# Kernel optimization log

Hardware: AMD Instinct MI355X
Metric: run time of the kernel (lower is better)

Reference implementation:

```python
import jax, jax.numpy as jnp
import numpy as np

N_NODES = 50000
N_EDGES = 800000
IN_DIM = 512
HID = 128
HEADS = 8
HEAD_DIM = HID // HEADS  # 16
N_LAYERS = 3
N_CLASSES = 8


def layer_norm(x, g, b, eps=1e-5):
    mu = jnp.mean(x, axis=-1, keepdims=True)
    var = jnp.mean((x - mu) ** 2, axis=-1, keepdims=True)
    return (x - mu) * jax.lax.rsqrt(var + eps) * g + b


def gat_layer(h, W, a_src, a_dst, bias, src, dst):
    # h: [N, HID]; W: [HID, HEADS*HEAD_DIM]; a_src/a_dst: [HEADS, HEAD_DIM]
    N = h.shape[0]
    hp = (h @ W).reshape(N, HEADS, HEAD_DIM)  # per-head projections
    e_s = jnp.einsum('nhc,hc->nh', hp, a_src)  # [N, H]
    e_d = jnp.einsum('nhc,hc->nh', hp, a_dst)
    logits = jax.nn.leaky_relu(e_s[src] + e_d[dst], negative_slope=0.2)  # [E, H]
    # segment softmax over incoming edges of each dst node
    m = jax.ops.segment_max(logits, dst, num_segments=N)
    p = jnp.exp(logits - m[dst])
    denom = jax.ops.segment_sum(p, dst, num_segments=N)
    alpha = p / (denom[dst] + 1e-16)  # [E, H]
    msg = hp[src] * alpha[:, :, None]  # [E, H, C]
    out = jax.ops.segment_sum(msg, dst, num_segments=N)  # [N, H, C]
    return out.reshape(N, HEADS * HEAD_DIM) + bias


def setup_inputs() -> dict:
    key = jax.random.key(0)
    ks = jax.random.split(key, 32)
    s = 0.05
    inp = {}
    inp['x'] = jax.random.normal(ks[0], (N_NODES, IN_DIM), dtype=jnp.float32)
    inp['edge_src'] = jax.random.randint(ks[1], (N_EDGES,), 0, N_NODES, dtype=jnp.int32)
    inp['edge_dst'] = jax.random.randint(ks[2], (N_EDGES,), 0, N_NODES, dtype=jnp.int32)
    # input projection
    inp['W_in'] = jax.random.normal(ks[3], (IN_DIM, HID)) * s
    inp['b_in'] = jnp.zeros((HID,))
    inp['g_in'] = jnp.ones((HID,))
    inp['be_in'] = jnp.zeros((HID,))
    # stacked GAT layer params
    inp['Wc'] = jax.random.normal(ks[4], (N_LAYERS, HID, HEADS * HEAD_DIM)) * s
    inp['a_src'] = jax.random.normal(ks[5], (N_LAYERS, HEADS, HEAD_DIM)) * s
    inp['a_dst'] = jax.random.normal(ks[6], (N_LAYERS, HEADS, HEAD_DIM)) * s
    inp['bc'] = jnp.zeros((N_LAYERS, HID))
    inp['gc'] = jnp.ones((N_LAYERS, HID))
    inp['bec'] = jnp.zeros((N_LAYERS, HID))
    # classifier
    inp['W1'] = jax.random.normal(ks[7], (HID, HID // 2)) * s
    inp['b1'] = jnp.zeros((HID // 2,))
    inp['g1'] = jnp.ones((HID // 2,))
    inp['be1'] = jnp.zeros((HID // 2,))
    inp['W2'] = jax.random.normal(ks[8], (HID // 2, HID // 4)) * s
    inp['b2'] = jnp.zeros((HID // 4,))
    inp['g2'] = jnp.ones((HID // 4,))
    inp['be2'] = jnp.zeros((HID // 4,))
    inp['W3'] = jax.random.normal(ks[9], (HID // 4, N_CLASSES)) * s
    inp['b3'] = jnp.zeros((N_CLASSES,))
    return inp


def reference(x, W_in, b_in, g_in, be_in, Wc, a_src, a_dst, bc, gc, bec,
              W1, b1, g1, be1, W2, b2, g2, be2, W3, b3, edge_src, edge_dst):
    N = x.shape[0]
    # PyG GATConv adds self-loops by default
    loops = jnp.arange(N, dtype=edge_src.dtype)
    src = jnp.concatenate([edge_src, loops])
    dst = jnp.concatenate([edge_dst, loops])
    # input projection (dropout is identity in eval)
    h = jax.nn.relu(layer_norm(x @ W_in + b_in, g_in, be_in))
    for i in range(N_LAYERS):
        residual = h
        h = gat_layer(h, Wc[i], a_src[i], a_dst[i], bc[i], src, dst)
        h = jax.nn.relu(layer_norm(h, gc[i], bec[i]))
        if i > 0:
            h = h + residual
    # classifier head
    h = jax.nn.relu(layer_norm(h @ W1 + b1, g1, be1))
    h = jax.nn.relu(layer_norm(h @ W2 + b2, g2, be2))
    return h @ W3 + b3
```

## Files before the change

### kernel.cpp

```cpp
#include <hip/hip_runtime.h>
#include <math.h>

#define N_NODES 50000
#define N_EDGES 800000
#define IN_DIM 512
#define HID 128
#define HEADS 8
#define HEAD_DIM 16
#define N_LAYERS 3
#define N_CLASSES 8
#define LOG2E 1.4426950408889634f
#define NBLK 196

typedef __attribute__((ext_vector_type(8))) short short8;
typedef __attribute__((ext_vector_type(4))) short short4v;
typedef __attribute__((ext_vector_type(4))) float f32x4;

__device__ inline unsigned short f2bf(float f) {
  unsigned u = __float_as_uint(f);
  u = (u + 0x7fffu + ((u >> 16) & 1u)) >> 16;
  return (unsigned short)u;
}
__device__ inline float bflo(unsigned u) { return __uint_as_float(u << 16); }
__device__ inline float bfhi(unsigned u) { return __uint_as_float(u & 0xffff0000u); }

__global__ __launch_bounds__(256) void k_prep(
    const float* __restrict__ W_in, const float* __restrict__ Wc,
    const float* __restrict__ W1, const float* __restrict__ W2,
    const float* __restrict__ W3,
    unsigned short* __restrict__ Wt_in, unsigned short* __restrict__ Wt_c,
    unsigned short* __restrict__ W1t, unsigned short* __restrict__ W2t,
    unsigned short* __restrict__ W3t, int* __restrict__ degcur) {
  int i = blockIdx.x * blockDim.x + threadIdx.x;
  if (i < 2 * N_NODES) degcur[i] = 0;
  if (i < IN_DIM * HID) {
    int c = i >> 9, k = i & 511;
    Wt_in[i] = f2bf(W_in[k * HID + c]);
  }
  if (i < N_LAYERS * HID * HID) {
    int l = i >> 14, r = i & 16383, c = r >> 7, k = r & 127;
    Wt_c[i] = f2bf(Wc[l * HID * HID + k * HID + c]);
  }
  if (i < 64 * 128) {
    int c = i >> 7, k = i & 127;
    W1t[i] = f2bf(W1[k * 64 + c]);
  }
  if (i < 32 * 64) {
    int c = i >> 6, k = i & 63;
    W2t[i] = f2bf(W2[k * 32 + c]);
  }
  if (i < 16 * 32) {
    int c = i >> 5, k = i & 31;
    W3t[i] = (c < 8) ? f2bf(W3[k * N_CLASSES + c]) : 0;
  }
}

template <int K>
__device__ inline void gemm_mainloop(const float* __restrict__ A, size_t row0,
                                     const unsigned short* __restrict__ Wt,
                                     unsigned short* lds_a, unsigned short* lds_b,
                                     f32x4 acc[8]) {
  const int tid = threadIdx.x;
  const int lane = tid & 63, wid = tid >> 6;
#pragma unroll
  for (int f = 0; f < 8; ++f)
#pragma unroll
    for (int j = 0; j < 4; ++j) acc[f][j] = 0.f;

  for (int kb = 0; kb < K; kb += 64) {
#pragma unroll
    for (int j = 0; j < 4; ++j) {
      int i = tid + j * 256;
      int r = i >> 4, kq = (i & 15) * 4;
      size_t rg = row0 + r;
      if (rg >= N_NODES) rg = N_NODES - 1;
      float4 v = *(const float4*)(A + rg * K + kb + kq);
      short4v b4;
      b4[0] = (short)f2bf(v.x); b4[1] = (short)f2bf(v.y);
      b4[2] = (short)f2bf(v.z); b4[3] = (short)f2bf(v.w);
      int idx = (r * 64 + kq) ^ ((r & 7) << 3);
      *(short4v*)&lds_a[idx] = b4;
    }
#pragma unroll
    for (int j = 0; j < 4; ++j) {
      int i = tid + j * 256;
      int c = i >> 3, kq = (i & 7) * 8;
      short8 w = *(const short8*)(Wt + (size_t)c * K + kb + kq);
      int idx = (c * 64 + kq) ^ ((c & 7) << 3);
      *(short8*)&lds_b[idx] = w;
    }
    __syncthreads();

    int arow = wid * 16 + (lane & 15);
    int kq8 = (lane >> 4) * 8;
    short8 a0 = *(short8*)&lds_a[(arow * 64 + kq8) ^ ((arow & 7) << 3)];
    short8 a1 = *(short8*)&lds_a[(arow * 64 + 32 + kq8) ^ ((arow & 7) << 3)];
#pragma unroll
    for (int f = 0; f < 8; ++f) {
      int c = f * 16 + (lane & 15);
      short8 b0 = *(short8*)&lds_b[(c * 64 + kq8) ^ ((c & 7) << 3)];
      short8 b1 = *(short8*)&lds_b[(c * 64 + 32 + kq8) ^ ((c & 7) << 3)];
      acc[f] = __builtin_amdgcn_mfma_f32_16x16x32_bf16(a0, b0, acc[f], 0, 0, 0);
      acc[f] = __builtin_amdgcn_mfma_f32_16x16x32_bf16(a1, b1, acc[f], 0, 0, 0);
    }
    __syncthreads();
  }
}

__global__ __launch_bounds__(256) void k_gemm_in(
    const float* __restrict__ x, const unsigned short* __restrict__ Wt,
    const float* __restrict__ b, const float* __restrict__ g,
    const float* __restrict__ be, float* __restrict__ h0) {
  __shared__ unsigned short lds_a[64 * 64];
  __shared__ unsigned short lds_b[128 * 64];
  f32x4 acc[8];
  size_t row0 = (size_t)blockIdx.x * 64;
  gemm_mainloop<IN_DIM>(x, row0, Wt, lds_a, lds_b, acc);

  int lane = threadIdx.x & 63, wid = threadIdx.x >> 6;
  int cbase = lane & 15;
  float s[4] = {0.f, 0.f, 0.f, 0.f}, q[4] = {0.f, 0.f, 0.f, 0.f};
  float gg[8], bb[8];
#pragma unroll
  for (int f = 0; f < 8; ++f) {
    int c = f * 16 + cbase;
    float bias = b[c];
    gg[f] = g[c]; bb[f] = be[c];
#pragma unroll
    for (int j = 0; j < 4; ++j) {
      float v = acc[f][j] + bias;
      acc[f][j] = v;
      s[j] += v; q[j] += v * v;
    }
  }
#pragma unroll
  for (int off = 8; off >= 1; off >>= 1)
#pragma unroll
    for (int j = 0; j < 4; ++j) {
      s[j] += __shfl_xor(s[j], off);
      q[j] += __shfl_xor(q[j], off);
    }
#pragma unroll
  for (int j = 0; j < 4; ++j) {
    size_t row = row0 + wid * 16 + (lane >> 4) * 4 + j;
    if (row < N_NODES) {
      float mu = s[j] * (1.f / 128.f);
      float var = q[j] * (1.f / 128.f) - mu * mu;
      float rs = rsqrtf(var + 1e-5f);
#pragma unroll
      for (int f = 0; f < 8; ++f) {
        float y = (acc[f][j] - mu) * rs * gg[f] + bb[f];
        h0[row * HID + f * 16 + cbase] = fmaxf(y, 0.f);
      }
    }
  }
}

__global__ __launch_bounds__(256) void k_gemm_gat(
    const float* __restrict__ h, const unsigned short* __restrict__ Wt,
    const float* __restrict__ asrc, const float* __restrict__ adst,
    unsigned short* __restrict__ hp_bf, float* __restrict__ es,
    float* __restrict__ ed) {
  __shared__ unsigned short lds_a[64 * 64];
  __shared__ unsigned short lds_b[128 * 64];
  f32x4 acc[8];
  size_t row0 = (size_t)blockIdx.x * 64;
  gemm_mainloop<HID>(h, row0, Wt, lds_a, lds_b, acc);

  int lane = threadIdx.x & 63, wid = threadIdx.x >> 6;
  int cbase = lane & 15;
#pragma unroll
  for (int f = 0; f < 8; ++f) {
    float av = asrc[f * 16 + cbase], bv = adst[f * 16 + cbase];
    float eS[4], eD[4];
#pragma unroll
    for (int j = 0; j < 4; ++j) { eS[j] = acc[f][j] * av; eD[j] = acc[f][j] * bv; }
#pragma unroll
    for (int off = 8; off >= 1; off >>= 1)
#pragma unroll
      for (int j = 0; j < 4; ++j) {
        eS[j] += __shfl_xor(eS[j], off);
        eD[j] += __shfl_xor(eD[j], off);
      }
#pragma unroll
    for (int j = 0; j < 4; ++j) {
      size_t row = row0 + wid * 16 + (lane >> 4) * 4 + j;
      if (row < N_NODES) {
        hp_bf[row * HID + f * 16 + cbase] = f2bf(acc[f][j]);
        if (cbase == 0) {
          es[row * HEADS + f] = eS[j] * LOG2E;
          ed[row * HEADS + f] = eD[j] * LOG2E;
        }
      }
    }
  }
}

__global__ void k_count(const int* __restrict__ dst, int* __restrict__ deg) {
  int e = blockIdx.x * blockDim.x + threadIdx.x;
  if (e < N_EDGES) atomicAdd(&deg[dst[e]], 1);
}

__global__ __launch_bounds__(256) void k_scan_local(
    const int* __restrict__ deg, int* __restrict__ startv,
    int* __restrict__ blocksum) {
  __shared__ int wsum[4];
  int tid = threadIdx.x, lane = tid & 63, wid = tid >> 6;
  int n = blockIdx.x * 256 + tid;
  int d = (n < N_NODES) ? deg[n] : 0;
  int v = d;
#pragma unroll
  for (int off = 1; off < 64; off <<= 1) {
    int t = __shfl_up(v, off);
    if (lane >= off) v += t;
  }
  if (lane == 63) wsum[wid] = v;
  __syncthreads();
  int prefix = 0;
  for (int w = 0; w < wid; ++w) prefix += wsum[w];
  int excl = prefix + v - d;
  if (n < N_NODES) startv[n] = excl;
  if (tid == 255) blocksum[blockIdx.x] = excl + d;
}

__global__ __launch_bounds__(256) void k_scan_block(
    const int* __restrict__ blocksum, int* __restrict__ blockoffs) {
  __shared__ int wsum[4];
  int tid = threadIdx.x, lane = tid & 63, wid = tid >> 6;
  int d = (tid < NBLK) ? blocksum[tid] : 0;
  int v = d;
#pragma unroll
  for (int off = 1; off < 64; off <<= 1) {
    int t = __shfl_up(v, off);
    if (lane >= off) v += t;
  }
  if (lane == 63) wsum[wid] = v;
  __syncthreads();
  int prefix = 0;
  for (int w = 0; w < wid; ++w) prefix += wsum[w];
  if (tid < NBLK) blockoffs[tid] = prefix + v - d;
}

__global__ __launch_bounds__(256) void k_scan_add(
    int* __restrict__ startv, const int* __restrict__ blockoffs) {
  int n = blockIdx.x * blockDim.x + threadIdx.x;
  if (n < N_NODES) startv[n] += blockoffs[blockIdx.x];
}

__global__ void k_scatter(const int* __restrict__ src, const int* __restrict__ dst,
                          const int* __restrict__ start, int* __restrict__ cur,
                          int* __restrict__ col) {
  int e = blockIdx.x * blockDim.x + threadIdx.x;
  if (e < N_EDGES) {
    int d = dst[e];
    int pos = start[d] + atomicAdd(&cur[d], 1);
    col[pos] = src[e];
  }
}

__global__ __launch_bounds__(256) void k_gat_agg(
    const unsigned short* __restrict__ hp_bf, const float* __restrict__ es,
    const float* __restrict__ ed, const int* __restrict__ start,
    const int* __restrict__ deg, const int* __restrict__ col,
    const float* __restrict__ bc, const float* __restrict__ gc,
    const float* __restrict__ bec, const float* __restrict__ h_res,
    float* __restrict__ h_out, int use_res) {
  int lane = threadIdx.x & 63;
  int n = blockIdx.x * 4 + (threadIdx.x >> 6);
  if (n >= N_NODES) return;
  int head = lane >> 3;
  int sub = lane & 7;
  int hbase = head * 8;
  const unsigned* hpu = (const unsigned*)hp_bf;

  float edv = ed[(size_t)n * HEADS + head];
  float z0 = es[(size_t)n * HEADS + head] + edv;
  z0 = fmaxf(z0, 0.2f * z0);
  float p0 = exp2f(z0);
  unsigned su = hpu[(size_t)n * 64 + lane];

  float den0 = p0, ax0 = p0 * bflo(su), ay0 = p0 * bfhi(su);
  float den1 = 0.f, ax1 = 0.f, ay1 = 0.f;

  int s0 = start[n], s1 = s0 + deg[n];
  int nb = (s1 - s0) >> 3;
  int base = s0;
  int se = 0;
  float p = 0.f;
  if (nb > 0) {
    se = col[base + sub];
    float z = es[(size_t)se * HEADS + head] + edv;
    z = fmaxf(z, 0.2f * z);
    p = exp2f(z);
  }
  for (int t = 0; t < nb; ++t) {
    int seN = 0;
    bool more = (t + 1 < nb);
    if (more) seN = col[base + 8 + sub];
#pragma unroll
    for (int k = 0; k < 8; k += 2) {
      float pk0 = __shfl(p, hbase + k);
      float pk1 = __shfl(p, hbase + k + 1);
      int sk0 = __shfl(se, k);
      int sk1 = __shfl(se, k + 1);
      unsigned h0 = hpu[(size_t)sk0 * 64 + lane];
      unsigned h1 = hpu[(size_t)sk1 * 64 + lane];
      den0 += pk0;
      ax0 = fmaf(pk0, bflo(h0), ax0);
      ay0 = fmaf(pk0, bfhi(h0), ay0);
      den1 += pk1;
      ax1 = fmaf(pk1, bflo(h1), ax1);
      ay1 = fmaf(pk1, bfhi(h1), ay1);
    }
    if (more) {
      float zN = es[(size_t)seN * HEADS + head] + edv;
      zN = fmaxf(zN, 0.2f * zN);
      p = exp2f(zN);
      se = seN;
    }
    base += 8;
  }
  int rem = s1 - base;
  if (rem > 0) {
    int e = base + (sub < rem ? sub : rem - 1);
    int set = col[e];
    float z = es[(size_t)set * HEADS + head] + edv;
    z = fmaxf(z, 0.2f * z);
    float pt = (sub < rem) ? exp2f(z) : 0.f;
    for (int k = 0; k < rem; ++k) {
      float pk = __shfl(pt, hbase + k);
      int sk = __shfl(set, k);
      unsigned hk = hpu[(size_t)sk * 64 + lane];
      den0 += pk;
      ax0 = fmaf(pk, bflo(hk), ax0);
      ay0 = fmaf(pk, bfhi(hk), ay0);
    }
  }
  float den = den0 + den1 + 1e-16f;
  float rden = 1.f / den;
  float v0 = (ax0 + ax1) * rden + bc[2 * lane];
  float v1 = (ay0 + ay1) * rden + bc[2 * lane + 1];

  float s = v0 + v1, q = v0 * v0 + v1 * v1;
#pragma unroll
  for (int off = 32; off >= 1; off >>= 1) {
    s += __shfl_xor(s, off);
    q += __shfl_xor(q, off);
  }
  float mu = s * (1.f / 128.f);
  float var = q * (1.f / 128.f) - mu * mu;
  float rs = rsqrtf(var + 1e-5f);
  float y0 = fmaxf((v0 - mu) * rs * gc[2 * lane] + bec[2 * lane], 0.f);
  float y1 = fmaxf((v1 - mu) * rs * gc[2 * lane + 1] + bec[2 * lane + 1], 0.f);
  if (use_res) {
    float2 r = ((const float2*)h_res)[(size_t)n * 64 + lane];
    y0 += r.x; y1 += r.y;
  }
  ((float2*)h_out)[(size_t)n * 64 + lane] = make_float2(y0, y1);
}

__global__ __launch_bounds__(256) void k_head_mfma(
    const float* __restrict__ h,
    const unsigned short* __restrict__ W1t, const float* __restrict__ b1,
    const float* __restrict__ g1, const float* __restrict__ be1,
    const unsigned short* __restrict__ W2t, const float* __restrict__ b2,
    const float* __restrict__ g2, const float* __restrict__ be2,
    const unsigned short* __restrict__ W3t, const float* __restrict__ b3,
    float* __restrict__ out) {
  __shared__ unsigned short lds_a[64 * 128];
  __shared__ unsigned short lds_b1[64 * 128];
  __shared__ unsigned short lds_h1[64 * 64];
  __shared__ unsigned short lds_b2[32 * 64];
  __shared__ unsigned short lds_h2[64 * 32];
  __shared__ unsigned short lds_b3[16 * 32];
  int tid = threadIdx.x, lane = tid & 63, wid = tid >> 6;
  size_t row0 = (size_t)blockIdx.x * 64;

#pragma unroll
  for (int jj = 0; jj < 8; ++jj) {
    int i = tid + jj * 256;
    int r = i >> 5, kq = (i & 31) * 4;
    size_t rg = row0 + r;
    if (rg >= N_NODES) rg = N_NODES - 1;
    float4 v = *(const float4*)(h + rg * HID + kq);
    short4v b4;
    b4[0] = (short)f2bf(v.x); b4[1] = (short)f2bf(v.y);
    b4[2] = (short)f2bf(v.z); b4[3] = (short)f2bf(v.w);
    int idx = (r * 128 + kq) ^ ((r & 7) << 3);
    *(short4v*)&lds_a[idx] = b4;
  }
#pragma unroll
  for (int jj = 0; jj < 4; ++jj) {
    int i = tid + jj * 256;
    int c = i >> 4, kq = (i & 15) * 8;
    short8 w = *(const short8*)(W1t + c * 128 + kq);
    int idx = (c * 128 + kq) ^ ((c & 7) << 3);
    *(short8*)&lds_b1[idx] = w;
  }
  {
    int c = tid >> 3, kq = (tid & 7) * 8;
    if (c < 32) {
      short8 w = *(const short8*)(W2t + c * 64 + kq);
      int idx = (c * 64 + kq) ^ ((c & 7) << 3);
      *(short8*)&lds_b2[idx] = w;
    }
  }
  if (tid < 64) {
    int c = tid >> 2, kq = (tid & 3) * 8;
    short8 w = *(const short8*)(W3t + c * 32 + kq);
    int idx = (c * 32 + kq) ^ ((c & 3) << 3);
    *(short8*)&lds_b3[idx] = w;
  }
  __syncthreads();

  int arow = wid * 16 + (lane & 15);
  int kq8 = (lane >> 4) * 8;
  int cbase = lane & 15;

  f32x4 acc1[4];
#pragma unroll
  for (int f = 0; f < 4; ++f)
#pragma unroll
    for (int j = 0; j < 4; ++j) acc1[f][j] = 0.f;
  {
    short8 a0 = *(short8*)&lds_a[(arow * 128 + kq8) ^ ((arow & 7) << 3)];
    short8 a1 = *(short8*)&lds_a[(arow * 128 + 32 + kq8) ^ ((arow & 7) << 3)];
    short8 a2 = *(short8*)&lds_a[(arow * 128 + 64 + kq8) ^ ((arow & 7) << 3)];
    short8 a3 = *(short8*)&lds_a[(arow * 128 + 96 + kq8) ^ ((arow & 7) << 3)];
#pragma unroll
    for (int f = 0; f < 4; ++f) {
      int c = f * 16 + cbase;
      short8 b0 = *(short8*)&lds_b1[(c * 128 + kq8) ^ ((c & 7) << 3)];
      short8 bb1 = *(short8*)&lds_b1[(c * 128 + 32 + kq8) ^ ((c & 7) << 3)];
      short8 b2v = *(short8*)&lds_b1[(c * 128 + 64 + kq8) ^ ((c & 7) << 3)];
      short8 b3v = *(short8*)&lds_b1[(c * 128 + 96 + kq8) ^ ((c & 7) << 3)];
      acc1[f] = __builtin_amdgcn_mfma_f32_16x16x32_bf16(a0, b0, acc1[f], 0, 0, 0);
      acc1[f] = __builtin_amdgcn_mfma_f32_16x16x32_bf16(a1, bb1, acc1[f], 0, 0, 0);
      acc1[f] = __builtin_amdgcn_mfma_f32_16x16x32_bf16(a2, b2v, acc1[f], 0, 0, 0);
      acc1[f] = __builtin_amdgcn_mfma_f32_16x16x32_bf16(a3, b3v, acc1[f], 0, 0, 0);
    }
  }
  {
    float s[4] = {0, 0, 0, 0}, q[4] = {0, 0, 0, 0};
#pragma unroll
    for (int f = 0; f < 4; ++f) {
      int c = f * 16 + cbase;
      float bias = b1[c];
#pragma unroll
      for (int j = 0; j < 4; ++j) {
        float v = acc1[f][j] + bias;
        acc1[f][j] = v;
        s[j] += v; q[j] += v * v;
      }
    }
#pragma unroll
    for (int off = 8; off >= 1; off >>= 1)
#pragma unroll
      for (int j = 0; j < 4; ++j) {
        s[j] += __shfl_xor(s[j], off);
        q[j] += __shfl_xor(q[j], off);
      }
#pragma unroll
    for (int j = 0; j < 4; ++j) {
      int row = wid * 16 + (lane >> 4) * 4 + j;
      float mu = s[j] * (1.f / 64.f);
      float var = q[j] * (1.f / 64.f) - mu * mu;
      float rs = rsqrtf(var + 1e-5f);
#pragma unroll
      for (int f = 0; f < 4; ++f) {
        int c = f * 16 + cbase;
        float y = fmaxf((acc1[f][j] - mu) * rs * g1[c] + be1[c], 0.f);
        lds_h1[(row * 64 + c) ^ ((row & 7) << 3)] = f2bf(y);
      }
    }
  }
  __syncthreads();

  f32x4 acc2[2];
#pragma unroll
  for (int f = 0; f < 2; ++f)
#pragma unroll
    for (int j = 0; j < 4; ++j) acc2[f][j] = 0.f;
  {
    short8 a0 = *(short8*)&lds_h1[(arow * 64 + kq8) ^ ((arow & 7) << 3)];
    short8 a1 = *(short8*)&lds_h1[(arow * 64 + 32 + kq8) ^ ((arow & 7) << 3)];
#pragma unroll
    for (int f = 0; f < 2; ++f) {
      int c = f * 16 + cbase;
      short8 b0 = *(short8*)&lds_b2[(c * 64 + kq8) ^ ((c & 7) << 3)];
      short8 bb1 = *(short8*)&lds_b2[(c * 64 + 32 + kq8) ^ ((c & 7) << 3)];
      acc2[f] = __builtin_amdgcn_mfma_f32_16x16x32_bf16(a0, b0, acc2[f], 0, 0, 0);
      acc2[f] = __builtin_amdgcn_mfma_f32_16x16x32_bf16(a1, bb1, acc2[f], 0, 0, 0);
    }
  }
  {
    float s[4] = {0, 0, 0, 0}, q[4] = {0, 0, 0, 0};
#pragma unroll
    for (int f = 0; f < 2; ++f) {
      int c = f * 16 + cbase;
      float bias = b2[c];
#pragma unroll
      for (int j = 0; j < 4; ++j) {
        float v = acc2[f][j] + bias;
        acc2[f][j] = v;
        s[j] += v; q[j] += v * v;
      }
    }
#pragma unroll
    for (int off = 8; off >= 1; off >>= 1)
#pragma unroll
      for (int j = 0; j < 4; ++j) {
        s[j] += __shfl_xor(s[j], off);
        q[j] += __shfl_xor(q[j], off);
      }
#pragma unroll
    for (int j = 0; j < 4; ++j) {
      int row = wid * 16 + (lane >> 4) * 4 + j;
      float mu = s[j] * (1.f / 32.f);
      float var = q[j] * (1.f / 32.f) - mu * mu;
      float rs = rsqrtf(var + 1e-5f);
#pragma unroll
      for (int f = 0; f < 2; ++f) {
        int c = f * 16 + cbase;
        float y = fmaxf((acc2[f][j] - mu) * rs * g2[c] + be2[c], 0.f);
        lds_h2[(row * 32 + c) ^ ((row & 3) << 3)] = f2bf(y);
      }
    }
  }
  __syncthreads();

  f32x4 acc3;
#pragma unroll
  for (int j = 0; j < 4; ++j) acc3[j] = 0.f;
  {
    short8 a = *(short8*)&lds_h2[(arow * 32 + kq8) ^ ((arow & 3) << 3)];
    short8 b = *(short8*)&lds_b3[(cbase * 32 + kq8) ^ ((cbase & 3) << 3)];
    acc3 = __builtin_amdgcn_mfma_f32_16x16x32_bf16(a, b, acc3, 0, 0, 0);
  }
  if (cbase < N_CLASSES) {
    float bias = b3[cbase];
#pragma unroll
    for (int j = 0; j < 4; ++j) {
      size_t row = row0 + wid * 16 + (lane >> 4) * 4 + j;
      if (row < N_NODES) out[row * N_CLASSES + cbase] = acc3[j] + bias;
    }
  }
}

extern "C" void kernel_launch(void* const* d_in, const int* in_sizes, int n_in,
                              void* d_out, int out_size, void* d_ws, size_t ws_size,
                              hipStream_t stream) {
  const float* x     = (const float*)d_in[0];
  const int*   esrc  = (const int*)d_in[1];
  const int*   edst  = (const int*)d_in[2];
  const float* W_in  = (const float*)d_in[3];
  const float* b_in  = (const float*)d_in[4];
  const float* g_in  = (const float*)d_in[5];
  const float* be_in = (const float*)d_in[6];
  const float* Wc    = (const float*)d_in[7];
  const float* a_src = (const float*)d_in[8];
  const float* a_dst = (const float*)d_in[9];
  const float* bc    = (const float*)d_in[10];
  const float* gc    = (const float*)d_in[11];
  const float* bec   = (const float*)d_in[12];
  const float* W1    = (const float*)d_in[13];
  const float* b1    = (const float*)d_in[14];
  const float* g1    = (const float*)d_in[15];
  const float* be1   = (const float*)d_in[16];
  const float* W2    = (const float*)d_in[17];
  const float* b2    = (const float*)d_in[18];
  const float* g2    = (const float*)d_in[19];
  const float* be2   = (const float*)d_in[20];
  const float* W3    = (const float*)d_in[21];
  const float* b3    = (const float*)d_in[22];

  float* ws = (float*)d_ws;
  const size_t NH = (size_t)N_NODES * HID;
  float* hA = ws;
  float* hB = hA + NH;
  float* es = hB + NH;
  float* ed = es + (size_t)N_NODES * HEADS;
  unsigned short* hp_bf = (unsigned short*)(ed + (size_t)N_NODES * HEADS);
  int* deg    = (int*)(hp_bf + NH);
  int* cur    = deg + N_NODES;
  int* startv = cur + N_NODES;
  int* blocksum  = startv + N_NODES;
  int* blockoffs = blocksum + NBLK;
  int* col    = blockoffs + NBLK;
  uintptr_t wp = (uintptr_t)(col + N_EDGES);
  wp = (wp + 15) & ~(uintptr_t)15;
  unsigned short* Wt_in = (unsigned short*)wp;
  unsigned short* Wt_c  = Wt_in + (size_t)IN_DIM * HID;
  unsigned short* W1t   = Wt_c + (size_t)N_LAYERS * HID * HID;
  unsigned short* W2t   = W1t + 64 * 128;
  unsigned short* W3t   = W2t + 32 * 64;

  k_prep<<<(2 * N_NODES + 255) / 256, 256, 0, stream>>>(
      W_in, Wc, W1, W2, W3, Wt_in, Wt_c, W1t, W2t, W3t, deg);

  k_gemm_in<<<(N_NODES + 63) / 64, 256, 0, stream>>>(x, Wt_in, b_in, g_in, be_in, hA);

  k_count<<<(N_EDGES + 255) / 256, 256, 0, stream>>>(edst, deg);
  k_scan_local<<<NBLK, 256, 0, stream>>>(deg, startv, blocksum);
  k_scan_block<<<1, 256, 0, stream>>>(blocksum, blockoffs);
  k_scan_add<<<NBLK, 256, 0, stream>>>(startv, blockoffs);
  k_scatter<<<(N_EDGES + 255) / 256, 256, 0, stream>>>(esrc, edst, startv, cur, col);

  float* hcur = hA;
  float* hnext = hB;
  for (int l = 0; l < N_LAYERS; ++l) {
    k_gemm_gat<<<(N_NODES + 63) / 64, 256, 0, stream>>>(
        hcur, Wt_c + (size_t)l * HID * HID,
        a_src + (size_t)l * HEADS * HEAD_DIM, a_dst + (size_t)l * HEADS * HEAD_DIM,
        hp_bf, es, ed);
    k_gat_agg<<<(N_NODES + 3) / 4, 256, 0, stream>>>(
        hp_bf, es, ed, startv, deg, col,
        bc + (size_t)l * HID, gc + (size_t)l * HID, bec + (size_t)l * HID,
        hcur, hnext, l > 0 ? 1 : 0);
    float* t = hcur; hcur = hnext; hnext = t;
  }

  k_head_mfma<<<(N_NODES + 63) / 64, 256, 0, stream>>>(
      hcur, W1t, b1, g1, be1, W2t, b2, g2, be2, W3t, b3, (float*)d_out);
}
```

Before: 338.3 us.

## Store hidden activations in bf16 between layers instead of fp32

Hidden-state buffers hA/hB become bf16 instead of fp32. The input GEMM, GAT aggregation and residual path write and read packed bf16, and the GAT GEMM and classifier head load bf16 directly into LDS without converting. This halves the bytes moved for inter-layer activations and removes the per-load fp32-to-bf16 conversion. In exchange, the residual stream now carries bf16 rounding, which loses some precision.

```diff
diff --git a/kernel.cpp b/kernel.cpp
--- a/kernel.cpp
+++ b/kernel.cpp
@@ -55,8 +55,8 @@
   }
 }
 
-template <int K>
-__device__ inline void gemm_mainloop(const float* __restrict__ A, size_t row0,
+template <int K, bool ABF>
+__device__ inline void gemm_mainloop(const void* __restrict__ Av, size_t row0,
                                      const unsigned short* __restrict__ Wt,
                                      unsigned short* lds_a, unsigned short* lds_b,
                                      f32x4 acc[8]) {
@@ -68,18 +68,33 @@
     for (int j = 0; j < 4; ++j) acc[f][j] = 0.f;
 
   for (int kb = 0; kb < K; kb += 64) {
-#pragma unroll
-    for (int j = 0; j < 4; ++j) {
-      int i = tid + j * 256;
-      int r = i >> 4, kq = (i & 15) * 4;
-      size_t rg = row0 + r;
-      if (rg >= N_NODES) rg = N_NODES - 1;
-      float4 v = *(const float4*)(A + rg * K + kb + kq);
-      short4v b4;
-      b4[0] = (short)f2bf(v.x); b4[1] = (short)f2bf(v.y);
-      b4[2] = (short)f2bf(v.z); b4[3] = (short)f2bf(v.w);
-      int idx = (r * 64 + kq) ^ ((r & 7) << 3);
-      *(short4v*)&lds_a[idx] = b4;
+    if (ABF) {
+      const unsigned short* A = (const unsigned short*)Av;
+#pragma unroll
+      for (int j = 0; j < 2; ++j) {
+        int i = tid + j * 256;
+        int r = i >> 3, kq = (i & 7) * 8;
+        size_t rg = row0 + r;
+        if (rg >= N_NODES) rg = N_NODES - 1;
+        short8 v = *(const short8*)(A + rg * K + kb + kq);
+        int idx = (r * 64 + kq) ^ ((r & 7) << 3);
+        *(short8*)&lds_a[idx] = v;
+      }
+    } else {
+      const float* A = (const float*)Av;
+#pragma unroll
+      for (int j = 0; j < 4; ++j) {
+        int i = tid + j * 256;
+        int r = i >> 4, kq = (i & 15) * 4;
+        size_t rg = row0 + r;
+        if (rg >= N_NODES) rg = N_NODES - 1;
+        float4 v = *(const float4*)(A + rg * K + kb + kq);
+        short4v b4;
+        b4[0] = (short)f2bf(v.x); b4[1] = (short)f2bf(v.y);
+        b4[2] = (short)f2bf(v.z); b4[3] = (short)f2bf(v.w);
+        int idx = (r * 64 + kq) ^ ((r & 7) << 3);
+        *(short4v*)&lds_a[idx] = b4;
+      }
     }
 #pragma unroll
     for (int j = 0; j < 4; ++j) {
@@ -110,12 +125,12 @@
 __global__ __launch_bounds__(256) void k_gemm_in(
     const float* __restrict__ x, const unsigned short* __restrict__ Wt,
     const float* __restrict__ b, const float* __restrict__ g,
-    const float* __restrict__ be, float* __restrict__ h0) {
+    const float* __restrict__ be, unsigned short* __restrict__ h0) {
   __shared__ unsigned short lds_a[64 * 64];
   __shared__ unsigned short lds_b[128 * 64];
   f32x4 acc[8];
   size_t row0 = (size_t)blockIdx.x * 64;
-  gemm_mainloop<IN_DIM>(x, row0, Wt, lds_a, lds_b, acc);
+  gemm_mainloop<IN_DIM, false>(x, row0, Wt, lds_a, lds_b, acc);
 
   int lane = threadIdx.x & 63, wid = threadIdx.x >> 6;
   int cbase = lane & 15;
@@ -150,14 +165,14 @@
 #pragma unroll
       for (int f = 0; f < 8; ++f) {
         float y = (acc[f][j] - mu) * rs * gg[f] + bb[f];
-        h0[row * HID + f * 16 + cbase] = fmaxf(y, 0.f);
+        h0[row * HID + f * 16 + cbase] = f2bf(fmaxf(y, 0.f));
       }
     }
   }
 }
 
 __global__ __launch_bounds__(256) void k_gemm_gat(
-    const float* __restrict__ h, const unsigned short* __restrict__ Wt,
+    const unsigned short* __restrict__ h, const unsigned short* __restrict__ Wt,
     const float* __restrict__ asrc, const float* __restrict__ adst,
     unsigned short* __restrict__ hp_bf, float* __restrict__ es,
     float* __restrict__ ed) {
@@ -165,7 +180,7 @@
   __shared__ unsigned short lds_b[128 * 64];
   f32x4 acc[8];
   size_t row0 = (size_t)blockIdx.x * 64;
-  gemm_mainloop<HID>(h, row0, Wt, lds_a, lds_b, acc);
+  gemm_mainloop<HID, true>(h, row0, Wt, lds_a, lds_b, acc);
 
   int lane = threadIdx.x & 63, wid = threadIdx.x >> 6;
   int cbase = lane & 15;
@@ -263,8 +278,8 @@
     const float* __restrict__ ed, const int* __restrict__ start,
     const int* __restrict__ deg, const int* __restrict__ col,
     const float* __restrict__ bc, const float* __restrict__ gc,
-    const float* __restrict__ bec, const float* __restrict__ h_res,
-    float* __restrict__ h_out, int use_res) {
+    const float* __restrict__ bec, const unsigned* __restrict__ h_res,
+    unsigned* __restrict__ h_out, int use_res) {
   int lane = threadIdx.x & 63;
   int n = blockIdx.x * 4 + (threadIdx.x >> 6);
   if (n >= N_NODES) return;
@@ -353,14 +368,14 @@
   float y0 = fmaxf((v0 - mu) * rs * gc[2 * lane] + bec[2 * lane], 0.f);
   float y1 = fmaxf((v1 - mu) * rs * gc[2 * lane + 1] + bec[2 * lane + 1], 0.f);
   if (use_res) {
-    float2 r = ((const float2*)h_res)[(size_t)n * 64 + lane];
-    y0 += r.x; y1 += r.y;
-  }
-  ((float2*)h_out)[(size_t)n * 64 + lane] = make_float2(y0, y1);
+    unsigned r = h_res[(size_t)n * 64 + lane];
+    y0 += bflo(r); y1 += bfhi(r);
+  }
+  h_out[(size_t)n * 64 + lane] = (unsigned)f2bf(y0) | ((unsigned)f2bf(y1) << 16);
 }
 
 __global__ __launch_bounds__(256) void k_head_mfma(
-    const float* __restrict__ h,
+    const unsigned short* __restrict__ h,
     const unsigned short* __restrict__ W1t, const float* __restrict__ b1,
     const float* __restrict__ g1, const float* __restrict__ be1,
     const unsigned short* __restrict__ W2t, const float* __restrict__ b2,
@@ -377,17 +392,14 @@
   size_t row0 = (size_t)blockIdx.x * 64;
 
 #pragma unroll
-  for (int jj = 0; jj < 8; ++jj) {
+  for (int jj = 0; jj < 4; ++jj) {
     int i = tid + jj * 256;
-    int r = i >> 5, kq = (i & 31) * 4;
+    int r = i >> 4, kq = (i & 15) * 8;
     size_t rg = row0 + r;
     if (rg >= N_NODES) rg = N_NODES - 1;
-    float4 v = *(const float4*)(h + rg * HID + kq);
-    short4v b4;
-    b4[0] = (short)f2bf(v.x); b4[1] = (short)f2bf(v.y);
-    b4[2] = (short)f2bf(v.z); b4[3] = (short)f2bf(v.w);
+    short8 v = *(const short8*)(h + rg * HID + kq);
     int idx = (r * 128 + kq) ^ ((r & 7) << 3);
-    *(short4v*)&lds_a[idx] = b4;
+    *(short8*)&lds_a[idx] = v;
   }
 #pragma unroll
   for (int jj = 0; jj < 4; ++jj) {
@@ -574,14 +586,13 @@
   const float* W3    = (const float*)d_in[21];
   const float* b3    = (const float*)d_in[22];
 
-  float* ws = (float*)d_ws;
   const size_t NH = (size_t)N_NODES * HID;
-  float* hA = ws;
-  float* hB = hA + NH;
-  float* es = hB + NH;
+  unsigned short* hA = (unsigned short*)d_ws;
+  unsigned short* hB = hA + NH;
+  unsigned short* hp_bf = hB + NH;
+  float* es = (float*)(hp_bf + NH);
   float* ed = es + (size_t)N_NODES * HEADS;
-  unsigned short* hp_bf = (unsigned short*)(ed + (size_t)N_NODES * HEADS);
-  int* deg    = (int*)(hp_bf + NH);
+  int* deg    = (int*)(ed + (size_t)N_NODES * HEADS);
   int* cur    = deg + N_NODES;
   int* startv = cur + N_NODES;
   int* blocksum  = startv + N_NODES;
@@ -606,8 +617,8 @@
   k_scan_add<<<NBLK, 256, 0, stream>>>(startv, blockoffs);
   k_scatter<<<(N_EDGES + 255) / 256, 256, 0, stream>>>(esrc, edst, startv, cur, col);
 
-  float* hcur = hA;
-  float* hnext = hB;
+  unsigned short* hcur = hA;
+  unsigned short* hnext = hB;
   for (int l = 0; l < N_LAYERS; ++l) {
     k_gemm_gat<<<(N_NODES + 63) / 64, 256, 0, stream>>>(
         hcur, Wt_c + (size_t)l * HID * HID,
@@ -616,8 +627,8 @@
     k_gat_agg<<<(N_NODES + 3) / 4, 256, 0, stream>>>(
         hp_bf, es, ed, startv, deg, col,
         bc + (size_t)l * HID, gc + (size_t)l * HID, bec + (size_t)l * HID,
-        hcur, hnext, l > 0 ? 1 : 0);
-    float* t = hcur; hcur = hnext; hnext = t;
+        (const unsigned*)hcur, (unsigned*)hnext, l > 0 ? 1 : 0);
+    unsigned short* t = hcur; hcur = hnext; hnext = t;
   }
 
   k_head_mfma<<<(N_NODES + 63) / 64, 256, 0, stream>>>(
```

After: 331.1 us. -2.1%, faster.
